# Kernel tuning notes

Measured on AMD Instinct MI355X. Metric: run time of the kernel, lower is better.

The kernel has to match this reference:

```python
import jax, jax.numpy as jnp
import numpy as np

B, N, C = 32, 4097, 256  # N odd so threshold length (N+1)//2 == N//2+1 rfft bins
F = N // 2 + 1


def setup_inputs() -> dict:
    key = jax.random.key(0)
    k1, k2, k3, k4 = jax.random.split(key, 4)
    x_in = jax.random.normal(k1, (B, N, C), dtype=jnp.float32)
    # trunc_normal(std=0.02) ~ scaled normal for reference purposes
    complex_weight = jax.random.normal(k2, (C, 2), dtype=jnp.float32) * 0.02
    complex_weight_high = jax.random.normal(k3, (C, 2), dtype=jnp.float32) * 0.02
    threshold_param = jax.random.uniform(k4, (F,), dtype=jnp.float32)
    return {
        "x_in": x_in,
        "complex_weight": complex_weight,
        "complex_weight_high": complex_weight_high,
        "threshold_param": threshold_param,
    }


def reference(x_in, complex_weight, complex_weight_high, threshold_param):
    dtype = x_in.dtype
    x = x_in.astype(jnp.float32)
    x_fft = jnp.fft.rfft(x, axis=1, norm="ortho")  # [B, F, C] complex64

    weight = complex_weight[:, 0] + 1j * complex_weight[:, 1]  # [C]
    x_weighted = x_fft * weight

    # adaptive high-frequency mask (straight-through on threshold_param)
    energy = jnp.sum(jnp.abs(x_fft) ** 2, axis=-1)  # [B, F]
    median_energy = jnp.median(energy, axis=1, keepdims=True)  # [B, 1] (F odd -> exact middle, matches torch)
    normalized_energy = energy / (median_energy + 1e-6)
    hard = (normalized_energy > threshold_param).astype(jnp.float32)  # [B, F]
    adaptive_mask = jax.lax.stop_gradient(hard - threshold_param) + threshold_param

    weight_high = complex_weight_high[:, 0] + 1j * complex_weight_high[:, 1]  # [C]
    x_weighted = x_weighted + x_fft * adaptive_mask[..., None] * weight_high

    out = jnp.fft.irfft(x_weighted, n=N, axis=1, norm="ortho")  # [B, N, C]
    return out.astype(dtype)
```

## Files before the change

### kernel.cpp

```cpp
#include <hip/hip_runtime.h>
#include <math.h>
#include <float.h>

#define B_ 32
#define N_ 4097
#define C_ 256
#define F_ 2049
#define N2_ 241
#define Q_ 512
#define TWROWS 4352
#define INV_SQRT_N 0.0156230927f
#define W_N 0.0015336063f
#define W_17 0.36959913571644626f

typedef __attribute__((ext_vector_type(8))) short short8v;
typedef _Float16 f16x8 __attribute__((ext_vector_type(8)));
typedef __attribute__((ext_vector_type(4))) float f32x4;

__device__ __forceinline__ float bf2f(unsigned short u) {
    return __uint_as_float(((unsigned)u) << 16);
}
__device__ __forceinline__ unsigned short f2bf(float v) {
    unsigned u = __float_as_uint(v);
    u += 0x7FFFu + ((u >> 16) & 1u);
    return (unsigned short)(u >> 16);
}
__device__ __forceinline__ unsigned short f2h(float v) {
    union { _Float16 h; unsigned short u; } cv;
    cv.h = (_Float16)v;
    return cv.u;
}
__device__ __forceinline__ void gload16(const void* gptr, void* ldsptr) {
    __builtin_amdgcn_global_load_lds(
        (const __attribute__((address_space(1))) void*)gptr,
        (__attribute__((address_space(3))) void*)ldsptr,
        16, 0, 0);
}

__global__ __launch_bounds__(256) void k_stageA_t(const float* __restrict__ x,
                                                  unsigned short* __restrict__ yt) {
    int bid = blockIdx.x;
    int b = bid >> 5; int rem = bid & 31;
    int n2t = rem >> 2, ct = rem & 3;
    int tid = threadIdx.x;
    int cl = tid & 63, sub = tid >> 6;
    int c = ct * 64 + cl;

    float C17[17], S17[17];
#pragma unroll
    for (int r = 0; r < 17; ++r) {
        float s, cth; sincosf(W_17 * (float)r, &s, &cth);
        C17[r] = cth; S17[r] = s;
    }

    float ar[9][8], ai[8][8];
#pragma unroll
    for (int k = 0; k < 9; ++k)
#pragma unroll
        for (int i = 0; i < 8; ++i) ar[k][i] = 0.f;
#pragma unroll
    for (int k = 0; k < 8; ++k)
#pragma unroll
        for (int i = 0; i < 8; ++i) ai[k][i] = 0.f;

    const float* xb = x + (size_t)b * N_ * C_ + c;
#pragma unroll
    for (int n1 = 0; n1 < 17; ++n1) {
        float xv[8];
#pragma unroll
        for (int i = 0; i < 8; ++i) {
            int n2 = n2t * 32 + sub * 8 + i;
            xv[i] = (n2 <= 240) ? xb[(size_t)(n1 * N2_ + n2) * C_] : 0.f;
        }
#pragma unroll
        for (int k1 = 0; k1 < 9; ++k1) {
            int r = (k1 * n1) % 17;
            float cc = C17[r], ss = S17[r];
#pragma unroll
            for (int i = 0; i < 8; ++i) {
                ar[k1][i] += xv[i] * cc;
                if (k1 > 0) ai[k1 - 1][i] += xv[i] * ss;
            }
        }
    }

    __shared__ float lre[32 * 65], lim[32 * 65];
    int c2 = tid >> 2, qg = tid & 3;
#pragma unroll
    for (int j = 0; j < 9; ++j) {
        __syncthreads();
#pragma unroll
        for (int i = 0; i < 8; ++i) {
            int row = sub * 8 + i;
            lre[row * 65 + cl] = ar[j][i] * INV_SQRT_N;
            lim[row * 65 + cl] = (j > 0) ? (-ai[j - 1][i] * INV_SQRT_N) : 0.f;
        }
        __syncthreads();
        unsigned wh[8];
#pragma unroll
        for (int i = 0; i < 8; ++i) {
            int row = qg * 8 + i;
            float re = lre[row * 65 + c2], im = lim[row * 65 + c2];
            wh[i] = (unsigned)f2h(re) | ((unsigned)f2h(im) << 16);
        }
        size_t ubase = ((size_t)((b * 9 + j) * 256 + ct * 64 + c2)) * 256 + n2t * 32 + qg * 8;
        uint4 v0; v0.x = wh[0]; v0.y = wh[1]; v0.z = wh[2]; v0.w = wh[3];
        uint4 v1; v1.x = wh[4]; v1.y = wh[5]; v1.z = wh[6]; v1.w = wh[7];
        *(uint4*)((unsigned*)yt + ubase) = v0;
        *(uint4*)((unsigned*)yt + ubase + 4) = v1;
    }
}

__global__ __launch_bounds__(256) void k_twfill_all(unsigned short* __restrict__ twA,
                                                    unsigned short* __restrict__ twB) {
    int blk = blockIdx.x;
    if (blk < TWROWS) {
        int n = blk;
        int k2 = threadIdx.x;
        unsigned pack = 0u;
        if (n <= 4096 && k2 <= 240) {
            int rr = (n * k2) % N_;
            float s, cth; sincosf(W_N * (float)rr, &s, &cth);
            pack = (unsigned)f2bf(cth) | ((unsigned)f2bf(-s) << 16);
        }
        *(unsigned*)(twA + (size_t)n * Q_ + 2 * k2) = pack;
    } else {
        int idx = blk - TWROWS;
        int m = idx & 255; int k1 = idx >> 8;
        int n2 = threadIdx.x;
        int t = m >> 1, r = m & 1;
        int f = k1 + 17 * t;
        unsigned ph = 0u;
        if (t <= 120 && f < F_ && n2 <= 240) {
            float s_ = (k1 <= 8) ? 1.f : -1.f;
            int rr = (f * n2) % N_;
            float sn, cs; sincosf(W_N * (float)rr, &sn, &cs);
            float a0 = (r == 0) ? cs : -sn;
            float a1 = (r == 0) ? s_ * sn : s_ * cs;
            ph = (unsigned)f2h(a0) | ((unsigned)f2h(a1) << 16);
        }
        size_t ub = ((size_t)(k1 * 256 + m)) * 256 + n2;
        *((unsigned*)twB + ub) = ph;
    }
}

__global__ __launch_bounds__(256) void k_stageB_v5(
        const unsigned short* __restrict__ yt, const unsigned short* __restrict__ twb,
        unsigned short* __restrict__ X, float* __restrict__ energy) {
    int bid = (blockIdx.x & 7) * 272 + (blockIdx.x >> 3);
    int b = bid / 68, rem = bid % 68;
    int j, mt, ct;
    if (rem < 4) { j = 0; mt = rem >> 1; ct = rem & 1; }
    else { int r2 = rem - 4; j = 1 + (r2 >> 3); int sub = r2 & 7; mt = sub >> 1; ct = sub & 1; }
    int k1 = (mt < 2) ? j : 17 - j;
    int mh = mt & 1;
    const unsigned short* pA = twb + (size_t)(k1 * 256 + mh * 128) * Q_;
    const unsigned short* pB = yt + (size_t)((b * 9 + j) * 256 + ct * 128) * Q_;

    int tid = threadIdx.x, lane = tid & 63, wid = tid >> 6;
    int wr = wid >> 1, wc = wid & 1;
    int l15 = lane & 15, lg = lane >> 4;
    int srow = lane >> 2, sch = lane & 3;

    __shared__ __align__(16) unsigned short lds[2][8192];
    __shared__ float eL[2][2][4][4][2];

    const unsigned short* gsrc[4];
#pragma unroll
    for (int r = 0; r < 4; ++r) {
        int row = (r & 1) * 64 + wid * 16 + srow;
        int ch = sch ^ ((row >> 1) & 3);
        gsrc[r] = ((r < 2) ? pA : pB) + (size_t)row * Q_ + ch * 8;
    }
    int aoff[4], boff[4];
#pragma unroll
    for (int rt = 0; rt < 4; ++rt) {
        int row = wr * 64 + rt * 16 + l15;
        aoff[rt] = row * 32 + (lg ^ ((row >> 1) & 3)) * 8;
    }
#pragma unroll
    for (int nt = 0; nt < 4; ++nt) {
        int row = wc * 64 + nt * 16 + l15;
        boff[nt] = 4096 + row * 32 + (lg ^ ((row >> 1) & 3)) * 8;
    }

    f32x4 acc[4][4];
#pragma unroll
    for (int rt = 0; rt < 4; ++rt)
#pragma unroll
        for (int nt = 0; nt < 4; ++nt) acc[rt][nt] = (f32x4){0.f, 0.f, 0.f, 0.f};

#define STAGE_B(bufi, q0) do {                                      \
        gload16(gsrc[0] + (q0), &lds[bufi][wid * 512]);             \
        gload16(gsrc[1] + (q0), &lds[bufi][2048 + wid * 512]);      \
        gload16(gsrc[2] + (q0), &lds[bufi][4096 + wid * 512]);      \
        gload16(gsrc[3] + (q0), &lds[bufi][6144 + wid * 512]);      \
    } while (0)

#define COMP_B(bufi) do {                                           \
        f16x8 a_[4], b_[4];                                         \
        _Pragma("unroll")                                           \
        for (int rt = 0; rt < 4; ++rt)                              \
            a_[rt] = *(const f16x8*)&lds[bufi][aoff[rt]];           \
        _Pragma("unroll")                                           \
        for (int nt = 0; nt < 4; ++nt)                              \
            b_[nt] = *(const f16x8*)&lds[bufi][boff[nt]];           \
        _Pragma("unroll")                                           \
        for (int rt = 0; rt < 4; ++rt)                              \
            _Pragma("unroll")                                       \
            for (int nt = 0; nt < 4; ++nt)                          \
                acc[rt][nt] = __builtin_amdgcn_mfma_f32_16x16x32_f16( \
                    a_[rt], b_[nt], acc[rt][nt], 0, 0, 0);          \
    } while (0)

    STAGE_B(0, 0);
    __syncthreads();
    for (int ks = 0; ks < 16; ks += 2) {
        STAGE_B(1, (ks + 1) * 32);
        COMP_B(0);
        __syncthreads();
        if (ks + 2 < 16) STAGE_B(0, (ks + 2) * 32);
        COMP_B(1);
        __syncthreads();
    }
#undef STAGE_B
#undef COMP_B

#pragma unroll
    for (int rt = 0; rt < 4; ++rt) {
        float e0 = 0.f, e1 = 0.f;
#pragma unroll
        for (int nt = 0; nt < 4; ++nt) {
            e0 += acc[rt][nt][0] * acc[rt][nt][0] + acc[rt][nt][1] * acc[rt][nt][1];
            e1 += acc[rt][nt][2] * acc[rt][nt][2] + acc[rt][nt][3] * acc[rt][nt][3];
        }
#pragma unroll
        for (int off = 1; off < 16; off <<= 1) {
            e0 += __shfl_xor(e0, off, 64);
            e1 += __shfl_xor(e1, off, 64);
        }
        if (l15 == 0) { eL[wr][wc][rt][lg][0] = e0; eL[wr][wc][rt][lg][1] = e1; }
    }
    __syncthreads();
    if (tid < 64) {
        int wr2 = tid >> 5, rt2 = (tid >> 3) & 3, lg2 = (tid >> 1) & 3, pr = tid & 1;
        int mrow = mh * 128 + wr2 * 64 + rt2 * 16 + lg2 * 4 + pr * 2;
        int f = k1 + 17 * (mrow >> 1);
        if (f < F_) {
            float e = eL[wr2][0][rt2][lg2][pr] + eL[wr2][1][rt2][lg2][pr];
            atomicAdd(&energy[b * F_ + f], e);
        }
    }

#pragma unroll
    for (int rt = 0; rt < 4; ++rt) {
#pragma unroll
        for (int jj = 0; jj < 4; ++jj) {
            int mrow = mh * 128 + wr * 64 + rt * 16 + lg * 4 + jj;
            int t = mrow >> 1, p = mrow & 1;
            int f = k1 + 17 * t;
            if (f < F_) {
                size_t base = ((size_t)((b * F_ + f) * 2 + p)) * C_ + ct * 128 + wc * 64 + l15;
#pragma unroll
                for (int nt = 0; nt < 4; ++nt)
                    X[base + nt * 16] = f2bf(acc[rt][nt][jj]);
            }
        }
    }
}

__global__ __launch_bounds__(256) void k_median(const float* __restrict__ energy,
                                                float* __restrict__ med) {
    int b = blockIdx.x, tid = threadIdx.x;
    __shared__ unsigned vals[F_];
    __shared__ unsigned hist[256];
    __shared__ unsigned scanbuf[256];
    __shared__ unsigned sh_prefix;
    __shared__ int sh_rank;
    for (int i = tid; i < F_; i += 256)
        vals[i] = __float_as_uint(energy[b * F_ + i]);
    if (tid == 0) { sh_prefix = 0u; sh_rank = 1024; }
    __syncthreads();
#pragma unroll
    for (int shift = 24; shift >= 0; shift -= 8) {
        hist[tid] = 0u;
        __syncthreads();
        unsigned prefix = sh_prefix;
        unsigned hmask = (shift == 24) ? 0u : (0xFFFFFFFFu << (shift + 8));
        for (int i = tid; i < F_; i += 256) {
            unsigned v = vals[i];
            if (((v ^ prefix) & hmask) == 0u)
                atomicAdd(&hist[(v >> shift) & 255], 1u);
        }
        __syncthreads();
        scanbuf[tid] = hist[tid];
        __syncthreads();
#pragma unroll
        for (int off = 1; off < 256; off <<= 1) {
            unsigned y = (tid >= off) ? scanbuf[tid - off] : 0u;
            __syncthreads();
            scanbuf[tid] += y;
            __syncthreads();
        }
        int rank = sh_rank;
        unsigned cumP = (tid == 0) ? 0u : scanbuf[tid - 1];
        unsigned cumI = scanbuf[tid];
        __syncthreads();
        if ((unsigned)rank >= cumP && (unsigned)rank < cumI) {
            sh_prefix = prefix | ((unsigned)tid << shift);
            sh_rank = rank - (int)cumP;
        }
        __syncthreads();
    }
    if (tid == 0) med[b] = __uint_as_float(sh_prefix);
}

__global__ __launch_bounds__(256) void k_vbuild_t(
        const unsigned short* __restrict__ X, const float* __restrict__ energy,
        const float* __restrict__ med, const float* __restrict__ thr,
        const float* __restrict__ cw, const float* __restrict__ cwh,
        unsigned short* __restrict__ vt) {
    int bid = blockIdx.x;
    int b = bid >> 7; int rem = bid & 127;
    int kt = rem >> 3, ct = rem & 7;
    int tid = threadIdx.x;
    int cl = tid & 31, ks = tid >> 5;
    int c = ct * 32 + cl;

    __shared__ unsigned stage[17 * 32 * 17];

    float wr = cw[2 * c], wi = cw[2 * c + 1];
    float whr = cwh[2 * c], whi = cwh[2 * c + 1];
    float denom = med[b] + 1e-6f;

    float C17[17], S17[17];
#pragma unroll
    for (int r = 0; r < 17; ++r) {
        float s, cth; sincosf(W_17 * (float)r, &s, &cth);
        C17[r] = cth; S17[r] = s;
    }

#pragma unroll
    for (int kk = 0; kk < 2; ++kk) {
        int klocal = kk * 8 + ks;
        int k2 = kt * 16 + klocal;
        float vr[17], vi[17];
#pragma unroll
        for (int m = 0; m < 17; ++m) { vr[m] = 0.f; vi[m] = 0.f; }
        if (k2 <= 240) {
#pragma unroll
            for (int s = 0; s < 9; ++s) {
                int f = k2 + 241 * s;
                if (f < F_) {
                    float e = energy[b * F_ + f];
                    float m = (e / denom > thr[f]) ? 1.0f : 0.0f;
                    float wer = wr + m * whr, wei = wi + m * whi;
                    float cf = ((f == 0) ? 1.0f : 2.0f) * INV_SQRT_N;
                    const unsigned short* Xrow = X + ((size_t)(b * F_ + f) * 2) * C_;
                    float Xr = bf2f(Xrow[c]), Xi = bf2f(Xrow[C_ + c]);
                    float Zr = (Xr * wer - Xi * wei) * cf;
                    float Zi = (Xr * wei + Xi * wer) * cf;
#pragma unroll
                    for (int m2 = 0; m2 < 17; ++m2) {
                        int r = (s * m2) % 17;
                        vr[m2] += Zr * C17[r] - Zi * S17[r];
                        vi[m2] += Zr * S17[r] + Zi * C17[r];
                    }
                }
            }
        }
#pragma unroll
        for (int m2 = 0; m2 < 17; ++m2)
            stage[(m2 * 32 + cl) * 17 + klocal] =
                (unsigned)f2bf(vr[m2]) | ((unsigned)f2bf(vi[m2]) << 16);
    }
    __syncthreads();
    unsigned* vt32 = (unsigned*)vt;
    for (int r = tid; r < 544; r += 256) {
        int m2 = r >> 5, c2 = r & 31;
        size_t ubase = ((size_t)((b * 17 + m2) * 256 + ct * 32 + c2)) * 256 + kt * 16;
        const unsigned* srow = &stage[(m2 * 32 + c2) * 17];
#pragma unroll
        for (int g = 0; g < 4; ++g) {
            uint4 w;
            w.x = srow[g * 4]; w.y = srow[g * 4 + 1];
            w.z = srow[g * 4 + 2]; w.w = srow[g * 4 + 3];
            *(uint4*)(vt32 + ubase + g * 4) = w;
        }
    }
}

__global__ __launch_bounds__(256) void k_stageC_v3(const short* __restrict__ vt,
                                                   const short* __restrict__ twA,
                                                   float* __restrict__ out) {
    int bid = (blockIdx.x & 7) * 272 + (blockIdx.x >> 3);
    int b = bid / 68, rem = bid % 68;
    int m2 = rem >> 2, mt = (rem >> 1) & 1, ct = rem & 1;

    int tid = threadIdx.x, lane = tid & 63, wid = tid >> 6;
    int wr = wid >> 1, wc = wid & 1;
    int l15 = lane & 15, lg = lane >> 4;
    int srow = lane >> 2, sch = lane & 3;

    const short* vtb = vt + (size_t)((b * 17 + m2) * 256 + ct * 128) * Q_;

    __shared__ __align__(16) short lds[2][8192];

    const short* gsrc[4];
#pragma unroll
    for (int r = 0; r < 4; ++r) {
        int row = (r & 1) * 64 + wid * 16 + srow;
        int ch = sch ^ ((row >> 1) & 3);
        if (r < 2) {
            int n = 17 * (mt * 128 + row) + m2;
            gsrc[r] = twA + (size_t)n * Q_ + ch * 8;
        } else {
            gsrc[r] = vtb + (size_t)row * Q_ + ch * 8;
        }
    }
    int aoff[4], boff[4];
#pragma unroll
    for (int rt = 0; rt < 4; ++rt) {
        int row = wr * 64 + rt * 16 + l15;
        aoff[rt] = row * 32 + (lg ^ ((row >> 1) & 3)) * 8;
    }
#pragma unroll
    for (int nt = 0; nt < 4; ++nt) {
        int row = wc * 64 + nt * 16 + l15;
        boff[nt] = 4096 + row * 32 + (lg ^ ((row >> 1) & 3)) * 8;
    }

    f32x4 acc[4][4];
#pragma unroll
    for (int rt = 0; rt < 4; ++rt)
#pragma unroll
        for (int nt = 0; nt < 4; ++nt) acc[rt][nt] = (f32x4){0.f, 0.f, 0.f, 0.f};

#define STAGE_C(bufi, q0) do {                                      \
        gload16(gsrc[0] + (q0), &lds[bufi][wid * 512]);             \
        gload16(gsrc[1] + (q0), &lds[bufi][2048 + wid * 512]);      \
        gload16(gsrc[2] + (q0), &lds[bufi][4096 + wid * 512]);      \
        gload16(gsrc[3] + (q0), &lds[bufi][6144 + wid * 512]);      \
    } while (0)

#define COMP_C(bufi) do {                                           \
        short8v a_[4], b_[4];                                       \
        _Pragma("unroll")                                           \
        for (int rt = 0; rt < 4; ++rt)                              \
            a_[rt] = *(const short8v*)&lds[bufi][aoff[rt]];         \
        _Pragma("unroll")                                           \
        for (int nt = 0; nt < 4; ++nt)                              \
            b_[nt] = *(const short8v*)&lds[bufi][boff[nt]];         \
        _Pragma("unroll")                                           \
        for (int rt = 0; rt < 4; ++rt)                              \
            _Pragma("unroll")                                       \
            for (int nt = 0; nt < 4; ++nt)                          \
                acc[rt][nt] = __builtin_amdgcn_mfma_f32_16x16x32_bf16( \
                    a_[rt], b_[nt], acc[rt][nt], 0, 0, 0);          \
    } while (0)

    STAGE_C(0, 0);
    __syncthreads();
    for (int ks = 0; ks < 16; ks += 2) {
        STAGE_C(1, (ks + 1) * 32);
        COMP_C(0);
        __syncthreads();
        if (ks + 2 < 16) STAGE_C(0, (ks + 2) * 32);
        COMP_C(1);
        __syncthreads();
    }
#undef STAGE_C
#undef COMP_C

#pragma unroll
    for (int rt = 0; rt < 4; ++rt) {
#pragma unroll
        for (int jj = 0; jj < 4; ++jj) {
            int m1 = mt * 128 + wr * 64 + rt * 16 + lg * 4 + jj;
            if (m1 < N2_) {
                int n = 17 * m1 + m2;
                float* orow = out + ((size_t)b * N_ + n) * C_ + ct * 128 + wc * 64;
#pragma unroll
                for (int nt = 0; nt < 4; ++nt)
                    orow[nt * 16 + l15] = acc[rt][nt][jj];
            }
        }
    }
}

extern "C" void kernel_launch(void* const* d_in, const int* in_sizes, int n_in,
                              void* d_out, int out_size, void* d_ws, size_t ws_size,
                              hipStream_t stream) {
    const float* x   = (const float*)d_in[0];
    const float* cw  = (const float*)d_in[1];
    const float* cwh = (const float*)d_in[2];
    const float* thr = (const float*)d_in[3];
    float* out = (float*)d_out;

    char* ws = (char*)d_ws;
    unsigned short* Xb    = (unsigned short*)ws;
    char* sh = ws + 67141632ull;
    unsigned short* yt    = (unsigned short*)sh;
    unsigned short* vtb   = (unsigned short*)sh;
    char* tail = sh + 142606336ull;
    unsigned short* twA   = (unsigned short*)tail;
    unsigned short* twB   = (unsigned short*)(tail + 4456448ull);
    float* energy = (float*)(tail + 8912896ull);
    float* med    = (float*)(tail + 8912896ull + 262272ull);

    hipMemsetAsync(energy, 0, B_ * F_ * sizeof(float), stream);
    k_twfill_all<<<TWROWS + 17 * 256, 256, 0, stream>>>(twA, twB);
    k_stageA_t<<<B_ * 32, 256, 0, stream>>>(x, yt);
    k_stageB_v5<<<B_ * 68, 256, 0, stream>>>(yt, twB, Xb, energy);
    k_median<<<B_, 256, 0, stream>>>(energy, med);
    k_vbuild_t<<<B_ * 128, 256, 0, stream>>>(Xb, energy, med, thr, cw, cwh, vtb);
    k_stageC_v3<<<B_ * 68, 256, 0, stream>>>((const short*)vtb, (const short*)twA, out);
}
```

Before: 303.0 us.

## Fuse twiddle fill into stage A, drop atomics and memset, coalesce epilogue stores

Merges the twiddle-table fill into the stage-A kernel as extra blocks, each handling four rows, which removes one launch. The energy atomicAdd and its memset are replaced by plain writes into two per-column-tile buffers that the median and vbuild kernels sum on read. The stage-B and stage-C epilogues now stage accumulators through LDS so each row goes out as a contiguous 4- or 8-byte-per-lane store instead of scattered 2- or 4-byte writes. The cost is extra LDS round trips and syncthreads in the epilogues, plus double energy reads downstream.

```diff
diff --git a/kernel.cpp b/kernel.cpp
--- a/kernel.cpp
+++ b/kernel.cpp
@@ -37,12 +37,50 @@
         16, 0, 0);
 }
 
-__global__ __launch_bounds__(256) void k_stageA_t(const float* __restrict__ x,
-                                                  unsigned short* __restrict__ yt) {
-    int bid = blockIdx.x;
-    int b = bid >> 5; int rem = bid & 31;
+__global__ __launch_bounds__(256) void k_prep(const float* __restrict__ x,
+                                              unsigned short* __restrict__ yt,
+                                              unsigned short* __restrict__ twA,
+                                              unsigned short* __restrict__ twB) {
+    int blk = blockIdx.x;
+    int tid = threadIdx.x;
+    if (blk >= 1024) {
+        int base = (blk - 1024) * 4;
+#pragma unroll
+        for (int u = 0; u < 4; ++u) {
+            int g = base + u;
+            if (g < TWROWS) {
+                int n = g, k2 = tid;
+                unsigned pack = 0u;
+                if (n <= 4096 && k2 <= 240) {
+                    int rr = (n * k2) % N_;
+                    float s, cth; sincosf(W_N * (float)rr, &s, &cth);
+                    pack = (unsigned)f2bf(cth) | ((unsigned)f2bf(-s) << 16);
+                }
+                *(unsigned*)(twA + (size_t)n * Q_ + 2 * k2) = pack;
+            } else {
+                int i2 = g - TWROWS;
+                int m = i2 & 255; int k1 = i2 >> 8;
+                int n2 = tid;
+                int t = m >> 1, r = m & 1;
+                int f = k1 + 17 * t;
+                unsigned ph = 0u;
+                if (t <= 120 && f < F_ && n2 <= 240) {
+                    float s_ = (k1 <= 8) ? 1.f : -1.f;
+                    int rr = (f * n2) % N_;
+                    float sn, cs; sincosf(W_N * (float)rr, &sn, &cs);
+                    float a0 = (r == 0) ? cs : -sn;
+                    float a1 = (r == 0) ? s_ * sn : s_ * cs;
+                    ph = (unsigned)f2h(a0) | ((unsigned)f2h(a1) << 16);
+                }
+                size_t ub = ((size_t)(k1 * 256 + m)) * 256 + n2;
+                *((unsigned*)twB + ub) = ph;
+            }
+        }
+        return;
+    }
+
+    int b = blk >> 5; int rem = blk & 31;
     int n2t = rem >> 2, ct = rem & 3;
-    int tid = threadIdx.x;
     int cl = tid & 63, sub = tid >> 6;
     int c = ct * 64 + cl;
 
@@ -111,42 +149,9 @@
     }
 }
 
-__global__ __launch_bounds__(256) void k_twfill_all(unsigned short* __restrict__ twA,
-                                                    unsigned short* __restrict__ twB) {
-    int blk = blockIdx.x;
-    if (blk < TWROWS) {
-        int n = blk;
-        int k2 = threadIdx.x;
-        unsigned pack = 0u;
-        if (n <= 4096 && k2 <= 240) {
-            int rr = (n * k2) % N_;
-            float s, cth; sincosf(W_N * (float)rr, &s, &cth);
-            pack = (unsigned)f2bf(cth) | ((unsigned)f2bf(-s) << 16);
-        }
-        *(unsigned*)(twA + (size_t)n * Q_ + 2 * k2) = pack;
-    } else {
-        int idx = blk - TWROWS;
-        int m = idx & 255; int k1 = idx >> 8;
-        int n2 = threadIdx.x;
-        int t = m >> 1, r = m & 1;
-        int f = k1 + 17 * t;
-        unsigned ph = 0u;
-        if (t <= 120 && f < F_ && n2 <= 240) {
-            float s_ = (k1 <= 8) ? 1.f : -1.f;
-            int rr = (f * n2) % N_;
-            float sn, cs; sincosf(W_N * (float)rr, &sn, &cs);
-            float a0 = (r == 0) ? cs : -sn;
-            float a1 = (r == 0) ? s_ * sn : s_ * cs;
-            ph = (unsigned)f2h(a0) | ((unsigned)f2h(a1) << 16);
-        }
-        size_t ub = ((size_t)(k1 * 256 + m)) * 256 + n2;
-        *((unsigned*)twB + ub) = ph;
-    }
-}
-
-__global__ __launch_bounds__(256) void k_stageB_v5(
+__global__ __launch_bounds__(256) void k_stageB_v6(
         const unsigned short* __restrict__ yt, const unsigned short* __restrict__ twb,
-        unsigned short* __restrict__ X, float* __restrict__ energy) {
+        unsigned short* __restrict__ X, float* __restrict__ e2) {
     int bid = (blockIdx.x & 7) * 272 + (blockIdx.x >> 3);
     int b = bid / 68, rem = bid % 68;
     int j, mt, ct;
@@ -248,28 +253,38 @@
         int f = k1 + 17 * (mrow >> 1);
         if (f < F_) {
             float e = eL[wr2][0][rt2][lg2][pr] + eL[wr2][1][rt2][lg2][pr];
-            atomicAdd(&energy[b * F_ + f], e);
-        }
-    }
-
+            e2[(size_t)ct * (B_ * F_) + b * F_ + f] = e;
+        }
+    }
+
+    unsigned short* st = (unsigned short*)lds;
 #pragma unroll
     for (int rt = 0; rt < 4; ++rt) {
-#pragma unroll
-        for (int jj = 0; jj < 4; ++jj) {
-            int mrow = mh * 128 + wr * 64 + rt * 16 + lg * 4 + jj;
+        __syncthreads();
+#pragma unroll
+        for (int nt = 0; nt < 4; ++nt)
+#pragma unroll
+            for (int jj = 0; jj < 4; ++jj) {
+                int ri = wr * 16 + lg * 4 + jj;
+                int col = wc * 64 + nt * 16 + l15;
+                st[ri * 132 + col] = f2bf(acc[rt][nt][jj]);
+            }
+        __syncthreads();
+#pragma unroll
+        for (int rr = 0; rr < 8; ++rr) {
+            int ri = wid * 8 + rr;
+            int mrow = mh * 128 + (ri >> 4) * 64 + rt * 16 + (ri & 15);
             int t = mrow >> 1, p = mrow & 1;
             int f = k1 + 17 * t;
             if (f < F_) {
-                size_t base = ((size_t)((b * F_ + f) * 2 + p)) * C_ + ct * 128 + wc * 64 + l15;
-#pragma unroll
-                for (int nt = 0; nt < 4; ++nt)
-                    X[base + nt * 16] = f2bf(acc[rt][nt][jj]);
-            }
-        }
-    }
-}
-
-__global__ __launch_bounds__(256) void k_median(const float* __restrict__ energy,
+                unsigned v = *(unsigned*)&st[ri * 132 + 2 * lane];
+                *(unsigned*)(X + ((size_t)((b * F_ + f) * 2 + p)) * C_ + ct * 128 + 2 * lane) = v;
+            }
+        }
+    }
+}
+
+__global__ __launch_bounds__(256) void k_median(const float* __restrict__ e2,
                                                 float* __restrict__ med) {
     int b = blockIdx.x, tid = threadIdx.x;
     __shared__ unsigned vals[F_];
@@ -278,7 +293,7 @@
     __shared__ unsigned sh_prefix;
     __shared__ int sh_rank;
     for (int i = tid; i < F_; i += 256)
-        vals[i] = __float_as_uint(energy[b * F_ + i]);
+        vals[i] = __float_as_uint(e2[b * F_ + i] + e2[(size_t)B_ * F_ + b * F_ + i]);
     if (tid == 0) { sh_prefix = 0u; sh_rank = 1024; }
     __syncthreads();
 #pragma unroll
@@ -316,7 +331,7 @@
 }
 
 __global__ __launch_bounds__(256) void k_vbuild_t(
-        const unsigned short* __restrict__ X, const float* __restrict__ energy,
+        const unsigned short* __restrict__ X, const float* __restrict__ e2,
         const float* __restrict__ med, const float* __restrict__ thr,
         const float* __restrict__ cw, const float* __restrict__ cwh,
         unsigned short* __restrict__ vt) {
@@ -352,7 +367,7 @@
             for (int s = 0; s < 9; ++s) {
                 int f = k2 + 241 * s;
                 if (f < F_) {
-                    float e = energy[b * F_ + f];
+                    float e = e2[b * F_ + f] + e2[(size_t)B_ * F_ + b * F_ + f];
                     float m = (e / denom > thr[f]) ? 1.0f : 0.0f;
                     float wer = wr + m * whr, wei = wi + m * whi;
                     float cf = ((f == 0) ? 1.0f : 2.0f) * INV_SQRT_N;
@@ -390,7 +405,7 @@
     }
 }
 
-__global__ __launch_bounds__(256) void k_stageC_v3(const short* __restrict__ vt,
+__global__ __launch_bounds__(256) void k_stageC_v4(const short* __restrict__ vt,
                                                    const short* __restrict__ twA,
                                                    float* __restrict__ out) {
     int bid = (blockIdx.x & 7) * 272 + (blockIdx.x >> 3);
@@ -472,17 +487,27 @@
 #undef STAGE_C
 #undef COMP_C
 
+    float* fl = (float*)lds;
 #pragma unroll
     for (int rt = 0; rt < 4; ++rt) {
-#pragma unroll
-        for (int jj = 0; jj < 4; ++jj) {
-            int m1 = mt * 128 + wr * 64 + rt * 16 + lg * 4 + jj;
+        __syncthreads();
+#pragma unroll
+        for (int nt = 0; nt < 4; ++nt)
+#pragma unroll
+            for (int jj = 0; jj < 4; ++jj) {
+                int ri = wr * 16 + lg * 4 + jj;
+                int col = wc * 64 + nt * 16 + l15;
+                fl[ri * 130 + col] = acc[rt][nt][jj];
+            }
+        __syncthreads();
+#pragma unroll
+        for (int rr = 0; rr < 8; ++rr) {
+            int ri = wid * 8 + rr;
+            int m1 = mt * 128 + (ri >> 4) * 64 + rt * 16 + (ri & 15);
             if (m1 < N2_) {
                 int n = 17 * m1 + m2;
-                float* orow = out + ((size_t)b * N_ + n) * C_ + ct * 128 + wc * 64;
-#pragma unroll
-                for (int nt = 0; nt < 4; ++nt)
-                    orow[nt * 16 + l15] = acc[rt][nt][jj];
+                float2 v = *(float2*)&fl[ri * 130 + 2 * lane];
+                *(float2*)(out + ((size_t)b * N_ + n) * C_ + ct * 128 + 2 * lane) = v;
             }
         }
     }
@@ -505,14 +530,12 @@
     char* tail = sh + 142606336ull;
     unsigned short* twA   = (unsigned short*)tail;
     unsigned short* twB   = (unsigned short*)(tail + 4456448ull);
-    float* energy = (float*)(tail + 8912896ull);
-    float* med    = (float*)(tail + 8912896ull + 262272ull);
-
-    hipMemsetAsync(energy, 0, B_ * F_ * sizeof(float), stream);
-    k_twfill_all<<<TWROWS + 17 * 256, 256, 0, stream>>>(twA, twB);
-    k_stageA_t<<<B_ * 32, 256, 0, stream>>>(x, yt);
-    k_stageB_v5<<<B_ * 68, 256, 0, stream>>>(yt, twB, Xb, energy);
-    k_median<<<B_, 256, 0, stream>>>(energy, med);
-    k_vbuild_t<<<B_ * 128, 256, 0, stream>>>(Xb, energy, med, thr, cw, cwh, vtb);
-    k_stageC_v3<<<B_ * 68, 256, 0, stream>>>((const short*)vtb, (const short*)twA, out);
-}
+    float* e2  = (float*)(tail + 8912896ull);
+    float* med = (float*)(tail + 8912896ull + 524544ull);
+
+    k_prep<<<3200, 256, 0, stream>>>(x, yt, twA, twB);
+    k_stageB_v6<<<B_ * 68, 256, 0, stream>>>(yt, twB, Xb, e2);
+    k_median<<<B_, 256, 0, stream>>>(e2, med);
+    k_vbuild_t<<<B_ * 128, 256, 0, stream>>>(Xb, e2, med, thr, cw, cwh, vtb);
+    k_stageC_v4<<<B_ * 68, 256, 0, stream>>>((const short*)vtb, (const short*)twA, out);
+}
```

Result: no change. 305.5 us (+0.9%).
